# Kernel optimization log

Measured on AMD Instinct MI355X. Metric: run time of the kernel, lower is better.

## Reference

```python
import jax, jax.numpy as jnp
import numpy as np


def setup_inputs() -> dict:
    key = jax.random.key(0)
    k1, k2 = jax.random.split(key)
    x = jax.random.normal(k1, (32, 128, 56, 56), dtype=jnp.float32)
    weight = jax.random.normal(k2, (256, 128, 3, 3), dtype=jnp.float32) * 0.01
    bias = jnp.zeros((256,), dtype=jnp.float32)
    return {"x": x, "weight": weight, "bias": bias}


def reference(x, weight, bias):
    # Faithful to Conv2dGEMM: im2col + GEMM is mathematically a standard
    # cross-correlation conv with the given stride/padding. We express it as
    # the efficient fused form (implicit GEMM) which computes identical math.
    stride, padding = 1, 1
    out = jax.lax.conv_general_dilated(
        x, weight,
        window_strides=(stride, stride),
        padding=[(padding, padding), (padding, padding)],
        dimension_numbers=("NCHW", "OIHW", "NCHW"),
    )  # [B, out_ch, H_out, W_out]
    return out + bias[None, :, None, None]
```

## Files before the change

kernel.cpp:

```cpp
#include <hip/hip_runtime.h>
#include <stdint.h>

typedef __bf16 bf16x8 __attribute__((ext_vector_type(8)));
typedef float  f32x4  __attribute__((ext_vector_type(4)));

#define NB   32
#define CI   128
#define HH   56
#define WW   56
#define CO   256
#define HP   58
#define HW   (HH*WW)
#define MTOT (NB*HW)
#define KTOT 1152

#define XT_ELEMS ((size_t)NB*HP*HP*CI)
#define XT_BYTES (XT_ELEMS*2)

__global__ void halo_zero(__bf16* __restrict__ xt) {
  int id = blockIdx.x * 256 + threadIdx.x;
  if (id >= NB * 228 * 16) return;
  int chunk = id & 15;
  int p = (id >> 4) % 228;
  int n = id / (228 * 16);
  int h, w;
  if (p < 58)       { h = 0;           w = p; }
  else if (p < 116) { h = 57;          w = p - 58; }
  else if (p < 172) { h = p - 116 + 1; w = 0; }
  else              { h = p - 172 + 1; w = 57; }
  int4* dst = (int4*)(xt + ((size_t)(n * HP + h) * HP + w) * CI) + chunk;
  *dst = make_int4(0, 0, 0, 0);
}

__global__ void xpose_kernel(const float* __restrict__ x, __bf16* __restrict__ xt) {
  int nh = blockIdx.x;
  int n = nh / HH, h = nh % HH;
  __shared__ float tile[CI][57];
  const float* src = x + (size_t)n * CI * HW + (size_t)h * WW;
  int t = threadIdx.x;
  for (int idx = t; idx < CI * 14; idx += 256) {
    int c = idx / 14, w4 = idx - c * 14;
    float4 v = *(const float4*)(src + (size_t)c * HW + w4 * 4);
    tile[c][w4 * 4 + 0] = v.x;
    tile[c][w4 * 4 + 1] = v.y;
    tile[c][w4 * 4 + 2] = v.z;
    tile[c][w4 * 4 + 3] = v.w;
  }
  __syncthreads();
  __bf16* dst = xt + ((size_t)(n * HP + h + 1) * HP + 1) * CI;
  for (int idx = t; idx < WW * 16; idx += 256) {
    int w = idx >> 4, c8 = (idx & 15) * 8;
    bf16x8 v;
    for (int k = 0; k < 8; ++k) v[k] = (__bf16)tile[c8 + k][w];
    *(bf16x8*)(dst + (size_t)w * CI + c8) = v;
  }
}

__global__ void wxform_kernel(const float* __restrict__ wg, __bf16* __restrict__ wt) {
  int id = blockIdx.x * 256 + threadIdx.x;
  int o = id / KTOT;
  int k = id - o * KTOT;
  int rs = k >> 7, c = k & 127;
  wt[id] = (__bf16)wg[(size_t)o * KTOT + c * 9 + rs];
}

#define BM 128
#define BN 128

__device__ __forceinline__ void gload_lds16(const __bf16* g, __bf16* l) {
  __builtin_amdgcn_global_load_lds(
      (const __attribute__((address_space(1))) void*)g,
      (__attribute__((address_space(3))) void*)l, 16, 0, 0);
}

__global__ __launch_bounds__(256, 3) void conv_gemm(
    const __bf16* __restrict__ xt, const __bf16* __restrict__ wt,
    const float* __restrict__ bias, float* __restrict__ out) {
  __shared__ __bf16 Alds[2][BM * 32];
  __shared__ __bf16 Blds[2][BN * 32];
  int t = threadIdx.x;
  int bx = blockIdx.x;
  int nb = bx & 1, mb = bx >> 1;

  size_t baseA[2], baseB[2];
  __bf16* ldsA[2][2];
  __bf16* ldsB[2][2];
  for (int i = 0; i < 2; ++i) {
    int ml = i * 64 + (t >> 2);
    unsigned m = mb * BM + ml;
    unsigned nimg = m / HW;
    unsigned hw = m - nimg * HW;
    unsigned h = hw / WW;
    unsigned w = hw - h * WW;
    baseA[i] = ((size_t)(nimg * HP + h) * HP + w) * CI + (t & 3) * 8;
    baseB[i] = (size_t)(nb * BN + ml) * KTOT + (t & 3) * 8;
    for (int p = 0; p < 2; ++p) {
      ldsA[i][p] = &Alds[p][ml * 32 + (t & 3) * 8];
      ldsB[i][p] = &Blds[p][ml * 32 + (t & 3) * 8];
    }
  }

  int wid = t >> 6, lane = t & 63;
  int wm = (wid >> 1) * 64, wn = (wid & 1) * 64;
  int lr = lane & 15, lk = (lane >> 4) * 8;

  f32x4 acc[4][4];
  for (int i = 0; i < 4; ++i)
    for (int j = 0; j < 4; ++j) acc[i][j] = (f32x4){0.f, 0.f, 0.f, 0.f};

  for (int kt = 0; kt < KTOT / 64; ++kt) {
    int rs = kt >> 1;
    int r = (rs * 11) >> 5;
    int s = rs - 3 * r;
    size_t offA = ((size_t)(r * HP + s)) * CI + (size_t)(kt & 1) * 64;
    size_t offB = (size_t)kt * 64;
    for (int p = 0; p < 2; ++p) {
      gload_lds16(xt + baseA[0] + offA + p * 32, ldsA[0][p]);
      gload_lds16(xt + baseA[1] + offA + p * 32, ldsA[1][p]);
      gload_lds16(wt + baseB[0] + offB + p * 32, ldsB[0][p]);
      gload_lds16(wt + baseB[1] + offB + p * 32, ldsB[1][p]);
    }
    __syncthreads();
    for (int p = 0; p < 2; ++p) {
      bf16x8 a[4], b[4];
      for (int i = 0; i < 4; ++i) {
        a[i] = *(const bf16x8*)&Alds[p][(wm + i * 16 + lr) * 32 + lk];
        b[i] = *(const bf16x8*)&Blds[p][(wn + i * 16 + lr) * 32 + lk];
      }
      for (int i = 0; i < 4; ++i)
        for (int j = 0; j < 4; ++j)
          acc[i][j] = __builtin_amdgcn_mfma_f32_16x16x32_bf16(a[i], b[j], acc[i][j], 0, 0, 0);
    }
    __syncthreads();
  }

  for (int j = 0; j < 4; ++j) {
    int o = nb * BN + wn + j * 16 + lr;
    float bv = bias[o];
    for (int i = 0; i < 4; ++i) {
      unsigned m0 = mb * BM + wm + i * 16 + (lane >> 4) * 4;
      for (int r2 = 0; r2 < 4; ++r2) {
        unsigned m = m0 + r2;
        unsigned nimg = m / HW;
        unsigned hw = m - nimg * HW;
        out[((size_t)nimg * CO + o) * HW + hw] = acc[i][j][r2] + bv;
      }
    }
  }
}

extern "C" void kernel_launch(void* const* d_in, const int* in_sizes, int n_in,
                              void* d_out, int out_size, void* d_ws, size_t ws_size,
                              hipStream_t stream) {
  const float* x    = (const float*)d_in[0];
  const float* wg   = (const float*)d_in[1];
  const float* bias = (const float*)d_in[2];
  float* out = (float*)d_out;

  __bf16* xt = (__bf16*)d_ws;
  __bf16* wt = (__bf16*)((char*)d_ws + XT_BYTES);

  halo_zero<<<(NB * 228 * 16 + 255) / 256, 256, 0, stream>>>(xt);
  xpose_kernel<<<NB * HH, 256, 0, stream>>>(x, xt);
  wxform_kernel<<<(CO * KTOT) / 256, 256, 0, stream>>>(wg, wt);
  conv_gemm<<<(MTOT / BM) * (CO / BN), 256, 0, stream>>>(xt, wt, bias, out);
}
```

Before: 225.0 us.

## Double-buffer GEMM K loop, fuse prep kernels, vectorize output stores

Restructures the conv GEMM main loop into a double-buffered pipeline over 32-wide K slices, prefetching the next slice into the alternate LDS buffer while computing on the current one, with a single barrier per step. Merges the halo-zero, input transpose and weight transform kernels into one launch to cut launch overhead. Output stores become 16-byte vector writes since four consecutive rows stay within one image. Smaller K steps mean more iterations and barriers, and overlap depends on how the compiler places waits for the async LDS loads.

```diff
diff --git a/kernel.cpp b/kernel.cpp
--- a/kernel.cpp
+++ b/kernel.cpp
@@ -17,55 +17,59 @@
 #define XT_ELEMS ((size_t)NB*HP*HP*CI)
 #define XT_BYTES (XT_ELEMS*2)
 
-__global__ void halo_zero(__bf16* __restrict__ xt) {
-  int id = blockIdx.x * 256 + threadIdx.x;
-  if (id >= NB * 228 * 16) return;
-  int chunk = id & 15;
-  int p = (id >> 4) % 228;
-  int n = id / (228 * 16);
-  int h, w;
-  if (p < 58)       { h = 0;           w = p; }
-  else if (p < 116) { h = 57;          w = p - 58; }
-  else if (p < 172) { h = p - 116 + 1; w = 0; }
-  else              { h = p - 172 + 1; w = 57; }
-  int4* dst = (int4*)(xt + ((size_t)(n * HP + h) * HP + w) * CI) + chunk;
-  *dst = make_int4(0, 0, 0, 0);
-}
-
-__global__ void xpose_kernel(const float* __restrict__ x, __bf16* __restrict__ xt) {
-  int nh = blockIdx.x;
-  int n = nh / HH, h = nh % HH;
+#define XPOSE_BLKS 1792
+#define WX_BLKS    1152
+#define HALO_BLKS  456
+__global__ void prep_kernel(const float* __restrict__ x, const float* __restrict__ wg,
+                            __bf16* __restrict__ xt, __bf16* __restrict__ wt) {
   __shared__ float tile[CI][57];
-  const float* src = x + (size_t)n * CI * HW + (size_t)h * WW;
+  int bid = blockIdx.x;
   int t = threadIdx.x;
-  for (int idx = t; idx < CI * 14; idx += 256) {
-    int c = idx / 14, w4 = idx - c * 14;
-    float4 v = *(const float4*)(src + (size_t)c * HW + w4 * 4);
-    tile[c][w4 * 4 + 0] = v.x;
-    tile[c][w4 * 4 + 1] = v.y;
-    tile[c][w4 * 4 + 2] = v.z;
-    tile[c][w4 * 4 + 3] = v.w;
+  if (bid < XPOSE_BLKS) {
+    int n = bid / HH, h = bid % HH;
+    const float* src = x + (size_t)n * CI * HW + (size_t)h * WW;
+    for (int idx = t; idx < CI * 14; idx += 256) {
+      int c = idx / 14, w4 = idx - c * 14;
+      float4 v = *(const float4*)(src + (size_t)c * HW + w4 * 4);
+      tile[c][w4 * 4 + 0] = v.x;
+      tile[c][w4 * 4 + 1] = v.y;
+      tile[c][w4 * 4 + 2] = v.z;
+      tile[c][w4 * 4 + 3] = v.w;
+    }
+    __syncthreads();
+    __bf16* dst = xt + ((size_t)(n * HP + h + 1) * HP + 1) * CI;
+    for (int idx = t; idx < WW * 16; idx += 256) {
+      int w = idx >> 4, c8 = (idx & 15) * 8;
+      bf16x8 v;
+      for (int k = 0; k < 8; ++k) v[k] = (__bf16)tile[c8 + k][w];
+      *(bf16x8*)(dst + (size_t)w * CI + c8) = v;
+    }
+  } else if (bid < XPOSE_BLKS + WX_BLKS) {
+    int id = (bid - XPOSE_BLKS) * 256 + t;
+    int o = id / KTOT;
+    int k = id - o * KTOT;
+    int rs = k >> 7, c = k & 127;
+    wt[id] = (__bf16)wg[(size_t)o * KTOT + c * 9 + rs];
+  } else {
+    int id = (bid - XPOSE_BLKS - WX_BLKS) * 256 + t;
+    if (id < NB * 228 * 16) {
+      int chunk = id & 15;
+      int p = (id >> 4) % 228;
+      int n = id / (228 * 16);
+      int h, w;
+      if (p < 58)       { h = 0;           w = p; }
+      else if (p < 116) { h = 57;          w = p - 58; }
+      else if (p < 172) { h = p - 116 + 1; w = 0; }
+      else              { h = p - 172 + 1; w = 57; }
+      int4* dst = (int4*)(xt + ((size_t)(n * HP + h) * HP + w) * CI) + chunk;
+      *dst = make_int4(0, 0, 0, 0);
+    }
   }
-  __syncthreads();
-  __bf16* dst = xt + ((size_t)(n * HP + h + 1) * HP + 1) * CI;
-  for (int idx = t; idx < WW * 16; idx += 256) {
-    int w = idx >> 4, c8 = (idx & 15) * 8;
-    bf16x8 v;
-    for (int k = 0; k < 8; ++k) v[k] = (__bf16)tile[c8 + k][w];
-    *(bf16x8*)(dst + (size_t)w * CI + c8) = v;
-  }
-}
-
-__global__ void wxform_kernel(const float* __restrict__ wg, __bf16* __restrict__ wt) {
-  int id = blockIdx.x * 256 + threadIdx.x;
-  int o = id / KTOT;
-  int k = id - o * KTOT;
-  int rs = k >> 7, c = k & 127;
-  wt[id] = (__bf16)wg[(size_t)o * KTOT + c * 9 + rs];
 }
 
 #define BM 128
 #define BN 128
+#define NKIT 36
 
 __device__ __forceinline__ void gload_lds16(const __bf16* g, __bf16* l) {
   __builtin_amdgcn_global_load_lds(
@@ -108,30 +112,36 @@
   for (int i = 0; i < 4; ++i)
     for (int j = 0; j < 4; ++j) acc[i][j] = (f32x4){0.f, 0.f, 0.f, 0.f};
 
-  for (int kt = 0; kt < KTOT / 64; ++kt) {
-    int rs = kt >> 1;
-    int r = (rs * 11) >> 5;
-    int s = rs - 3 * r;
-    size_t offA = ((size_t)(r * HP + s)) * CI + (size_t)(kt & 1) * 64;
-    size_t offB = (size_t)kt * 64;
-    for (int p = 0; p < 2; ++p) {
-      gload_lds16(xt + baseA[0] + offA + p * 32, ldsA[0][p]);
-      gload_lds16(xt + baseA[1] + offA + p * 32, ldsA[1][p]);
-      gload_lds16(wt + baseB[0] + offB + p * 32, ldsB[0][p]);
-      gload_lds16(wt + baseB[1] + offB + p * 32, ldsB[1][p]);
+  gload_lds16(xt + baseA[0], ldsA[0][0]);
+  gload_lds16(xt + baseA[1], ldsA[1][0]);
+  gload_lds16(wt + baseB[0], ldsB[0][0]);
+  gload_lds16(wt + baseB[1], ldsB[1][0]);
+
+#pragma unroll 2
+  for (int kt = 0; kt < NKIT; ++kt) {
+    int cur = kt & 1;
+    __syncthreads();
+    if (kt != NKIT - 1) {
+      int kn = kt + 1;
+      int rs = kn >> 2;
+      int r = (rs * 11) >> 5;
+      int s = rs - 3 * r;
+      size_t offA = ((size_t)(r * HP + s)) * CI + (size_t)(kn & 3) * 32;
+      size_t offB = (size_t)kn * 32;
+      int nxt = cur ^ 1;
+      gload_lds16(xt + baseA[0] + offA, ldsA[0][nxt]);
+      gload_lds16(xt + baseA[1] + offA, ldsA[1][nxt]);
+      gload_lds16(wt + baseB[0] + offB, ldsB[0][nxt]);
+      gload_lds16(wt + baseB[1] + offB, ldsB[1][nxt]);
     }
-    __syncthreads();
-    for (int p = 0; p < 2; ++p) {
-      bf16x8 a[4], b[4];
-      for (int i = 0; i < 4; ++i) {
-        a[i] = *(const bf16x8*)&Alds[p][(wm + i * 16 + lr) * 32 + lk];
-        b[i] = *(const bf16x8*)&Blds[p][(wn + i * 16 + lr) * 32 + lk];
-      }
-      for (int i = 0; i < 4; ++i)
-        for (int j = 0; j < 4; ++j)
-          acc[i][j] = __builtin_amdgcn_mfma_f32_16x16x32_bf16(a[i], b[j], acc[i][j], 0, 0, 0);
+    bf16x8 a[4], b[4];
+    for (int i = 0; i < 4; ++i) {
+      a[i] = *(const bf16x8*)&Alds[cur][(wm + i * 16 + lr) * 32 + lk];
+      b[i] = *(const bf16x8*)&Blds[cur][(wn + i * 16 + lr) * 32 + lk];
     }
-    __syncthreads();
+    for (int i = 0; i < 4; ++i)
+      for (int j = 0; j < 4; ++j)
+        acc[i][j] = __builtin_amdgcn_mfma_f32_16x16x32_bf16(a[i], b[j], acc[i][j], 0, 0, 0);
   }
 
   for (int j = 0; j < 4; ++j) {
@@ -139,12 +149,10 @@
     float bv = bias[o];
     for (int i = 0; i < 4; ++i) {
       unsigned m0 = mb * BM + wm + i * 16 + (lane >> 4) * 4;
-      for (int r2 = 0; r2 < 4; ++r2) {
-        unsigned m = m0 + r2;
-        unsigned nimg = m / HW;
-        unsigned hw = m - nimg * HW;
-        out[((size_t)nimg * CO + o) * HW + hw] = acc[i][j][r2] + bv;
-      }
+      unsigned nimg = m0 / HW;
+      unsigned hw = m0 - nimg * HW;
+      f32x4 v = acc[i][j] + bv;
+      *(f32x4*)(out + ((size_t)nimg * CO + o) * HW + hw) = v;
     }
   }
 }
@@ -160,8 +168,6 @@
   __bf16* xt = (__bf16*)d_ws;
   __bf16* wt = (__bf16*)((char*)d_ws + XT_BYTES);
 
-  halo_zero<<<(NB * 228 * 16 + 255) / 256, 256, 0, stream>>>(xt);
-  xpose_kernel<<<NB * HH, 256, 0, stream>>>(x, xt);
-  wxform_kernel<<<(CO * KTOT) / 256, 256, 0, stream>>>(wg, wt);
+  prep_kernel<<<XPOSE_BLKS + WX_BLKS + HALO_BLKS, 256, 0, stream>>>(x, wg, xt, wt);
   conv_gemm<<<(MTOT / BM) * (CO / BN), 256, 0, stream>>>(xt, wt, bias, out);
 }
```

Result: no change. 229.3 us (+1.9%).
